# Performance work log

Measured on AMD Instinct MI355X. Metric: run time of the kernel, lower is better.

The kernel has to match this reference:

```python
import jax, jax.numpy as jnp
import numpy as np

D_MODEL = 1024
NUM_HEADS = 16
D_K = D_MODEL // NUM_HEADS


def setup_inputs() -> dict:
    key = jax.random.key(0)
    ks = jax.random.split(key, 16)
    B, S, D = 4, 2048, D_MODEL
    scale = 1.0 / np.sqrt(D)
    inp = {
        'Xs': jax.random.normal(ks[0], (B, S, D), jnp.float32),
        'Xt': jax.random.normal(ks[1], (B, S, D), jnp.float32),
    }
    names = ['qs', 'qt', 'ks', 'kt', 'vs', 'vt']
    for i, n in enumerate(names):
        inp['W_' + n] = jax.random.normal(ks[2 + 2 * i], (D, D), jnp.float32) * scale
        inp['b_' + n] = jax.random.normal(ks[3 + 2 * i], (D,), jnp.float32) * 0.01
    inp['attn_bias'] = jnp.zeros((1, 1, 1, 1), jnp.float32)
    return inp


def _split_heads(x):
    B, S, _ = x.shape
    return x.reshape(B, S, NUM_HEADS, D_K).transpose(0, 2, 1, 3)  # (B,H,S,dk)


def reference(Xs, Xt, W_qs, b_qs, W_qt, b_qt, W_ks, b_ks, W_kt, b_kt,
              W_vs, b_vs, W_vt, b_vt, attn_bias):
    # Dual-linear fused projections: Linear(x) = x @ W.T + b (torch convention)
    Q = Xs @ W_qs.T + b_qs + Xt @ W_qt.T + b_qt
    K = Xs @ W_ks.T + b_ks + Xt @ W_kt.T + b_kt
    V = Xs @ W_vs.T + b_vs + Xt @ W_vt.T + b_vt
    Q, K, V = _split_heads(Q), _split_heads(K), _split_heads(V)
    scores = jnp.einsum('bhqd,bhkd->bhqk', Q, K) / jnp.sqrt(jnp.float32(D_K))
    scores = scores + attn_bias  # scalar learned bias, broadcast
    probs = jax.nn.softmax(scores, axis=-1)
    out = jnp.einsum('bhqk,bhkd->bhqd', probs, V)  # (B,H,S,dk)
    B, H, S, dk = out.shape
    return out.transpose(0, 2, 1, 3).reshape(B, S, H * dk)
```

## Files before the change

kernel.cpp:

```cpp
#include <hip/hip_runtime.h>
#include <hip/hip_bf16.h>

typedef __bf16 bf16;
typedef __attribute__((ext_vector_type(8))) __bf16 bf16x8;
typedef __attribute__((ext_vector_type(4))) __bf16 bf16x4;
typedef __attribute__((ext_vector_type(4))) float f32x4;

#define D_MODEL 1024
#define NHEAD 16
#define DK 64
#define BB 4
#define SS 2048
#define MM 8192
#define KK 2048
#define NN 3072

#define LDP 72
#define QSCALE 0.18033688011112042f

__device__ __forceinline__ void glds16(const bf16* g, bf16* s) {
    __builtin_amdgcn_global_load_lds(
        (const __attribute__((address_space(1))) void*)g,
        (__attribute__((address_space(3))) void*)s, 16, 0, 0);
}

__device__ __forceinline__ void pack_group4(const float* __restrict__ srow,
                                            bf16* __restrict__ dst,
                                            int mt, int ktile, int mi, int g4) {
    const float4* s4 = (const float4*)&srow[g4 * 32];
    bf16x8 o[4];
#pragma unroll
    for (int q = 0; q < 4; ++q) {
        float4 v0 = s4[2 * q], v1 = s4[2 * q + 1];
        o[q][0]=(bf16)v0.x; o[q][1]=(bf16)v0.y; o[q][2]=(bf16)v0.z; o[q][3]=(bf16)v0.w;
        o[q][4]=(bf16)v1.x; o[q][5]=(bf16)v1.y; o[q][6]=(bf16)v1.z; o[q][7]=(bf16)v1.w;
    }
    const int s = mi & 7;
    const int chi = 4 * (g4 & 1);
    bf16* base = dst + (((((size_t)mt * 32 + ktile) << 10) + mi * 8) << 3);
#pragma unroll
    for (int q = 0; q < 4; ++q)
        *(bf16x8*)&base[((q + chi) ^ s) << 3] = o[q];
}

__global__ void pack_all(const float* __restrict__ Xs, const float* __restrict__ Xt,
                         const float* __restrict__ Wqs, const float* __restrict__ Wqt,
                         const float* __restrict__ Wks, const float* __restrict__ Wkt,
                         const float* __restrict__ Wvs, const float* __restrict__ Wvt,
                         const float* __restrict__ bqs, const float* __restrict__ bqt,
                         const float* __restrict__ bks, const float* __restrict__ bkt,
                         const float* __restrict__ bvs, const float* __restrict__ bvt,
                         bf16* __restrict__ Xp, bf16* __restrict__ Wp,
                         float* __restrict__ biasc) {
    int blk = blockIdx.x;
    if (blk < 2048) {
        int u = blk * 256 + threadIdx.x;
        int sel = u >> 18;
        int idx4 = u & 262143;
        int m = idx4 >> 5, g4 = idx4 & 31;
        const float* src = sel ? Xt : Xs;
        pack_group4(src + ((size_t)m << 10), Xp,
                    m >> 7, sel * 16 + (g4 >> 1), m & 127, g4);
        return;
    }
    if (blk < 2816) {
        int v = (blk - 2048) * 256 + threadIdx.x;
        int gi = v >> 15;
        int idx4 = v & 32767;
        int m = idx4 >> 5, g4 = idx4 & 31;
        const float* src = (gi == 0) ? Wqs : (gi == 1) ? Wqt : (gi == 2) ? Wks
                         : (gi == 3) ? Wkt : (gi == 4) ? Wvs : Wvt;
        pack_group4(src + ((size_t)m << 10), Wp,
                    (gi >> 1) * 8 + (m >> 7), (gi & 1) * 16 + (g4 >> 1),
                    m & 127, g4);
        return;
    }
    for (int n = threadIdx.x; n < NN; n += 256) {
        int g = n >> 10, c = n & 1023;
        const float* a = (g == 0) ? bqs : ((g == 1) ? bks : bvs);
        const float* b = (g == 0) ? bqt : ((g == 1) ? bkt : bvt);
        biasc[n] = a[c] + b[c];
    }
}

#define VM6 asm volatile("s_waitcnt vmcnt(6)" ::: "memory")
#define VM0 asm volatile("s_waitcnt vmcnt(0)" ::: "memory")
#define VMNONE
#define LGKM0 asm volatile("s_waitcnt lgkmcnt(0)" ::: "memory")

#define STG(gsrc, ldst) do {                                                  \
    glds16((gsrc) + ((size_t)t << 3), (ldst) + (w << 9));                     \
    glds16((gsrc) + (((size_t)t + 512) << 3), (ldst) + ((w + 8) << 9));       \
  } while (0)

#define TILE(P, KT, DO_STAGE, VMOP) do {                                      \
    const bf16* aP = &sA[P][wm << 6];                                         \
    const bf16* bP = &sB[P][bH][bR << 6];                                     \
    bf16x8 aF[4][2], bF[4][2];                                                \
    _Pragma("unroll")                                                         \
    for (int mi = 0; mi < 4; mi++)                                            \
      aF[mi][0] = *(const bf16x8*)&aP[((mi*16+l16)<<6) + ((quad^swz)<<3)];    \
    _Pragma("unroll")                                                         \
    for (int ni = 0; ni < 4; ni++)                                            \
      bF[ni][0] = *(const bf16x8*)&bP[((ni*16+l16)<<6) + ((quad^swz)<<3)];    \
    _Pragma("unroll")                                                         \
    for (int mi = 0; mi < 4; mi++)                                            \
      aF[mi][1] = *(const bf16x8*)&aP[((mi*16+l16)<<6) + (((4+quad)^swz)<<3)];\
    _Pragma("unroll")                                                         \
    for (int ni = 0; ni < 4; ni++)                                            \
      bF[ni][1] = *(const bf16x8*)&bP[((ni*16+l16)<<6) + (((4+quad)^swz)<<3)];\
    __builtin_amdgcn_s_setprio(1);                                            \
    _Pragma("unroll")                                                         \
    for (int mi = 0; mi < 4; mi++)                                            \
      _Pragma("unroll")                                                       \
      for (int ni = 0; ni < 4; ni++)                                          \
        acc[mi][ni] = __builtin_amdgcn_mfma_f32_16x16x32_bf16(                \
            aF[mi][0], bF[ni][0], acc[mi][ni], 0, 0, 0);                      \
    __builtin_amdgcn_s_setprio(0);                                            \
    LGKM0;                                                                    \
    __builtin_amdgcn_sched_barrier(0);                                        \
    __builtin_amdgcn_s_barrier();                                             \
    __builtin_amdgcn_sched_barrier(0);                                        \
    if (DO_STAGE) {                                                           \
      STG(Ag  + ((size_t)((KT) + 2) << 13), &sA[P][0]);                       \
      STG(Bg0 + ((size_t)((KT) + 2) << 13), &sB[P][0][0]);                    \
      STG(Bg1 + ((size_t)((KT) + 2) << 13), &sB[P][1][0]);                    \
    }                                                                         \
    __builtin_amdgcn_s_setprio(1);                                            \
    _Pragma("unroll")                                                         \
    for (int mi = 0; mi < 4; mi++)                                            \
      _Pragma("unroll")                                                       \
      for (int ni = 0; ni < 4; ni++)                                          \
        acc[mi][ni] = __builtin_amdgcn_mfma_f32_16x16x32_bf16(                \
            aF[mi][1], bF[ni][1], acc[mi][ni], 0, 0, 0);                      \
    __builtin_amdgcn_s_setprio(0);                                            \
    VMOP;                                                                     \
    __builtin_amdgcn_s_barrier();                                             \
    __builtin_amdgcn_sched_barrier(0);                                        \
  } while (0)

__global__ __launch_bounds__(512, 2) void gemm_qkv(
    const bf16* __restrict__ Xp, const bf16* __restrict__ Wp,
    const float* __restrict__ biasc,
    bf16* __restrict__ Qb, bf16* __restrict__ Kb, bf16* __restrict__ Vt) {
    __shared__ __align__(16) bf16 sA[2][8192];
    __shared__ __align__(16) bf16 sB[2][2][8192];

    const int t = threadIdx.x, lane = t & 63, w = t >> 6;
    const int quad = lane >> 4, l16 = lane & 15, swz = l16 & 7;
    const int wq = w & 3;
    const int wm = (w >> 2) * 64;
    const int wn = wq * 64;
    const int bH = wq >> 1;
    const int bR = (wq & 1) * 64;

    const int bx = blockIdx.x, by = blockIdx.y;
    const bf16* Ag  = Xp + (((size_t)bx * 32) << 13);
    const bf16* Bg0 = Wp + (((size_t)(by * 2 + 0) * 32) << 13);
    const bf16* Bg1 = Wp + (((size_t)(by * 2 + 1) * 32) << 13);

    f32x4 acc[4][4] = {};

    STG(Ag, &sA[0][0]); STG(Bg0, &sB[0][0][0]); STG(Bg1, &sB[0][1][0]);
    STG(Ag + 8192, &sA[1][0]); STG(Bg0 + 8192, &sB[1][0][0]); STG(Bg1 + 8192, &sB[1][1][0]);
    VM6;
    __builtin_amdgcn_s_barrier();
    __builtin_amdgcn_sched_barrier(0);

    int kt = 0;
#pragma unroll 1
    for (int i = 0; i < 15; i++, kt += 2) {
        TILE(0, kt, 1, VM6);
        TILE(1, kt + 1, 1, VM6);
    }
    TILE(0, 30, 0, VM0);
    TILE(1, 31, 0, VMNONE);

    const int g = by >> 2;
    const int m00 = bx << 7, n00 = by << 8;
#pragma unroll
    for (int mi = 0; mi < 4; mi++) {
        int mbase = m00 + wm + mi * 16 + quad * 4;
#pragma unroll
        for (int ni = 0; ni < 4; ni++) {
            int n = n00 + wn + ni * 16 + l16;
            float bias = biasc[n];
            int c = n & 1023, h = c >> 6, d = c & 63;
#pragma unroll
            for (int r = 0; r < 4; r++) {
                int m = mbase + r;
                int b = m >> 11, s = m & 2047;
                size_t bh = (size_t)(b * NHEAD + h);
                float v = acc[mi][ni][r] + bias;
                if (g == 0)
                    Qb[(bh * SS + s) * DK + d] = (bf16)(v * QSCALE);
                else if (g == 1)
                    Kb[(bh * SS + s) * DK + d] = (bf16)v;
                else
                    Vt[(bh * DK + d) * SS + s] = (bf16)v;
            }
        }
    }
}

__global__ __launch_bounds__(256) void attn(
    const bf16* __restrict__ Qb, const bf16* __restrict__ Kb,
    const bf16* __restrict__ Vt, float* __restrict__ out) {
    __shared__ __align__(16) bf16 sK[64 * 64];
    __shared__ __align__(16) bf16 sV[64 * 64];
    __shared__ __align__(16) bf16 sP[4][32 * LDP];

    const int lid = blockIdx.x + gridDim.x * blockIdx.y;
    const int bh = (lid & 7) * 8 + ((lid >> 3) & 7);
    const int q0 = (lid >> 6) * 128;

    const int t = threadIdx.x;
    const int lane = t & 63, w = t >> 6;
    const int quad = lane >> 4, l16 = lane & 15, swz = l16 & 7;
    const int b = bh >> 4, h = bh & 15;

    const bf16* Qp = Qb + ((size_t)bh * SS + q0 + w * 32) * DK;
    bf16x8 qf[2][2];
#pragma unroll
    for (int f = 0; f < 2; f++)
#pragma unroll
        for (int kb = 0; kb < 2; kb++)
            qf[f][kb] = *(const bf16x8*)&Qp[(f * 16 + l16) * DK + kb * 32 + quad * 8];

    f32x4 o[2][4] = {};
    float lsum[2] = {0.f, 0.f};

    const bf16* Kp = Kb + (size_t)bh * SS * DK;
    const bf16* Vp = Vt + (size_t)bh * DK * SS;

    for (int kt = 0; kt < SS; kt += 64) {
#pragma unroll
        for (int j = 0; j < 2; j++) {
            int u = (w * 2 + j) * 64 + lane;
            int row = u >> 3;
            int cc = (u & 7) ^ (row & 7);
            glds16(Kp + (size_t)(kt + row) * DK + cc * 8, &sK[(w * 2 + j) * 512]);
            glds16(Vp + (size_t)row * SS + kt + cc * 8, &sV[(w * 2 + j) * 512]);
        }
        __syncthreads();

        f32x4 st[2][4] = {};
#pragma unroll
        for (int kb = 0; kb < 2; kb++)
#pragma unroll
            for (int ki = 0; ki < 4; ki++) {
                bf16x8 kf = *(const bf16x8*)&sK[(ki * 16 + l16) * 64 + (((kb * 4 + quad) ^ swz) * 8)];
                st[0][ki] = __builtin_amdgcn_mfma_f32_16x16x32_bf16(kf, qf[0][kb], st[0][ki], 0, 0, 0);
                st[1][ki] = __builtin_amdgcn_mfma_f32_16x16x32_bf16(kf, qf[1][kb], st[1][ki], 0, 0, 0);
            }

#pragma unroll
        for (int f = 0; f < 2; f++) {
            float ls = 0.f;
#pragma unroll
            for (int ki = 0; ki < 4; ki++) {
                float p0 = __builtin_amdgcn_exp2f(st[f][ki][0]);
                float p1 = __builtin_amdgcn_exp2f(st[f][ki][1]);
                float p2 = __builtin_amdgcn_exp2f(st[f][ki][2]);
                float p3 = __builtin_amdgcn_exp2f(st[f][ki][3]);
                ls += (p0 + p1) + (p2 + p3);
                bf16x4 pk;
                pk[0] = (bf16)p0; pk[1] = (bf16)p1; pk[2] = (bf16)p2; pk[3] = (bf16)p3;
                *(bf16x4*)&sP[w][(f * 16 + l16) * LDP + ki * 16 + quad * 4] = pk;
            }
            lsum[f] += ls;
        }

#pragma unroll
        for (int kb = 0; kb < 2; kb++) {
            bf16x8 af0 = *(const bf16x8*)&sP[w][(l16) * LDP + kb * 32 + quad * 8];
            bf16x8 af1 = *(const bf16x8*)&sP[w][(16 + l16) * LDP + kb * 32 + quad * 8];
#pragma unroll
            for (int ni = 0; ni < 4; ni++) {
                bf16x8 vf = *(const bf16x8*)&sV[(ni * 16 + l16) * 64 + (((kb * 4 + quad) ^ swz) * 8)];
                o[0][ni] = __builtin_amdgcn_mfma_f32_16x16x32_bf16(af0, vf, o[0][ni], 0, 0, 0);
                o[1][ni] = __builtin_amdgcn_mfma_f32_16x16x32_bf16(af1, vf, o[1][ni], 0, 0, 0);
            }
        }
        __syncthreads();
    }

#pragma unroll
    for (int f = 0; f < 2; f++) {
        lsum[f] += __shfl_xor(lsum[f], 16);
        lsum[f] += __shfl_xor(lsum[f], 32);
    }

    float* op = out + ((size_t)(b * SS + q0 + w * 32)) * D_MODEL + h * DK;
#pragma unroll
    for (int f = 0; f < 2; f++)
#pragma unroll
        for (int r = 0; r < 4; r++) {
            float linv = 1.0f / __shfl(lsum[f], quad * 4 + r);
#pragma unroll
            for (int ni = 0; ni < 4; ni++)
                op[(f * 16 + quad * 4 + r) * D_MODEL + ni * 16 + l16] = o[f][ni][r] * linv;
        }
}

extern "C" void kernel_launch(void* const* d_in, const int* in_sizes, int n_in,
                              void* d_out, int out_size, void* d_ws, size_t ws_size,
                              hipStream_t stream) {
    const float* Xs   = (const float*)d_in[0];
    const float* Xt   = (const float*)d_in[1];
    const float* Wqs  = (const float*)d_in[2];
    const float* bqs  = (const float*)d_in[3];
    const float* Wqt  = (const float*)d_in[4];
    const float* bqt  = (const float*)d_in[5];
    const float* Wks  = (const float*)d_in[6];
    const float* bks  = (const float*)d_in[7];
    const float* Wkt  = (const float*)d_in[8];
    const float* bkt  = (const float*)d_in[9];
    const float* Wvs  = (const float*)d_in[10];
    const float* bvs  = (const float*)d_in[11];
    const float* Wvt  = (const float*)d_in[12];
    const float* bvt  = (const float*)d_in[13];
    float* out = (float*)d_out;

    char* ws = (char*)d_ws;
    bf16*  Xp    = (bf16*)(ws);
    bf16*  Wp    = (bf16*)(ws + 33554432);
    float* biasc = (float*)(ws + 46137344);
    bf16*  Qb    = (bf16*)(ws + 46149632);
    bf16*  Kb    = (bf16*)(ws + 62926848);
    bf16*  Vt    = (bf16*)(ws + 79704064);

    pack_all<<<2817, 256, 0, stream>>>(Xs, Xt, Wqs, Wqt, Wks, Wkt, Wvs, Wvt,
                                       bqs, bqt, bks, bkt, bvs, bvt,
                                       Xp, Wp, biasc);

    gemm_qkv<<<dim3(MM / 128, NN / 256), 512, 0, stream>>>(Xp, Wp, biasc, Qb, Kb, Vt);

    attn<<<dim3(SS / 128, BB * NHEAD), 256, 0, stream>>>(Qb, Kb, Vt, out);
}
```

Baseline: 369.8 us.

## Double-buffer K/V tiles in attention kernel to overlap loads with compute

Converts the attention loop's shared K and V tiles to a two-stage ping-pong buffer. The next tile is prefetched with direct-to-LDS global loads while the current tile feeds the MFMAs, and the trailing barrier is replaced by a vmcnt wait plus one barrier per iteration. The goal is to hide global-load latency behind compute. In exchange it doubles K/V LDS usage, which may reduce occupancy, and it depends on a VM0 wait macro defined elsewhere.

Result: slower. 380.9 us (+3.0%).

```diff
diff --git a/kernel.cpp b/kernel.cpp
--- a/kernel.cpp
+++ b/kernel.cpp
@@ -206,8 +206,8 @@
 __global__ __launch_bounds__(256) void attn(
     const bf16* __restrict__ Qb, const bf16* __restrict__ Kb,
     const bf16* __restrict__ Vt, float* __restrict__ out) {
-    __shared__ __align__(16) bf16 sK[64 * 64];
-    __shared__ __align__(16) bf16 sV[64 * 64];
+    __shared__ __align__(16) bf16 sK[2][64 * 64];
+    __shared__ __align__(16) bf16 sV[2][64 * 64];
     __shared__ __align__(16) bf16 sP[4][32 * LDP];
 
     const int lid = blockIdx.x + gridDim.x * blockIdx.y;
@@ -233,23 +233,40 @@
     const bf16* Kp = Kb + (size_t)bh * SS * DK;
     const bf16* Vp = Vt + (size_t)bh * DK * SS;
 
-    for (int kt = 0; kt < SS; kt += 64) {
-#pragma unroll
-        for (int j = 0; j < 2; j++) {
-            int u = (w * 2 + j) * 64 + lane;
-            int row = u >> 3;
-            int cc = (u & 7) ^ (row & 7);
-            glds16(Kp + (size_t)(kt + row) * DK + cc * 8, &sK[(w * 2 + j) * 512]);
-            glds16(Vp + (size_t)row * SS + kt + cc * 8, &sV[(w * 2 + j) * 512]);
-        }
-        __syncthreads();
+    const int u0 = (w * 2 + 0) * 64 + lane, u1 = u0 + 64;
+    const int r0 = u0 >> 3, c0 = (u0 & 7) ^ (r0 & 7);
+    const int r1 = u1 >> 3, c1 = (u1 & 7) ^ (r1 & 7);
+    const bf16* Kg0 = Kp + r0 * DK + c0 * 8;
+    const bf16* Kg1 = Kp + r1 * DK + c1 * 8;
+    const bf16* Vg0 = Vp + (size_t)r0 * SS + c0 * 8;
+    const bf16* Vg1 = Vp + (size_t)r1 * SS + c1 * 8;
+    const int ls0 = (w * 2 + 0) * 512, ls1 = (w * 2 + 1) * 512;
+
+#define ASTG(P, KT) do {                                                      \
+    glds16(Kg0 + (size_t)(KT) * 64, &sK[P][ls0]);                             \
+    glds16(Kg1 + (size_t)(KT) * 64, &sK[P][ls1]);                             \
+    glds16(Vg0 + (KT),              &sV[P][ls0]);                             \
+    glds16(Vg1 + (KT),              &sV[P][ls1]);                             \
+  } while (0)
+
+    ASTG(0, 0);
+
+#pragma unroll 1
+    for (int it = 0; it < 32; ++it) {
+        VM0;
+        __builtin_amdgcn_s_barrier();
+        __builtin_amdgcn_sched_barrier(0);
+        if (it < 31) ASTG((it + 1) & 1, (it + 1) * 64);
+
+        const bf16* kS = &sK[it & 1][0];
+        const bf16* vS = &sV[it & 1][0];
 
         f32x4 st[2][4] = {};
 #pragma unroll
         for (int kb = 0; kb < 2; kb++)
 #pragma unroll
             for (int ki = 0; ki < 4; ki++) {
-                bf16x8 kf = *(const bf16x8*)&sK[(ki * 16 + l16) * 64 + (((kb * 4 + quad) ^ swz) * 8)];
+                bf16x8 kf = *(const bf16x8*)&kS[(ki * 16 + l16) * 64 + (((kb * 4 + quad) ^ swz) * 8)];
                 st[0][ki] = __builtin_amdgcn_mfma_f32_16x16x32_bf16(kf, qf[0][kb], st[0][ki], 0, 0, 0);
                 st[1][ki] = __builtin_amdgcn_mfma_f32_16x16x32_bf16(kf, qf[1][kb], st[1][ki], 0, 0, 0);
             }
@@ -277,13 +294,13 @@
             bf16x8 af1 = *(const bf16x8*)&sP[w][(16 + l16) * LDP + kb * 32 + quad * 8];
 #pragma unroll
             for (int ni = 0; ni < 4; ni++) {
-                bf16x8 vf = *(const bf16x8*)&sV[(ni * 16 + l16) * 64 + (((kb * 4 + quad) ^ swz) * 8)];
+                bf16x8 vf = *(const bf16x8*)&vS[(ni * 16 + l16) * 64 + (((kb * 4 + quad) ^ swz) * 8)];
                 o[0][ni] = __builtin_amdgcn_mfma_f32_16x16x32_bf16(af0, vf, o[0][ni], 0, 0, 0);
                 o[1][ni] = __builtin_amdgcn_mfma_f32_16x16x32_bf16(af1, vf, o[1][ni], 0, 0, 0);
             }
         }
-        __syncthreads();
-    }
+    }
+#undef ASTG
 
 #pragma unroll
     for (int f = 0; f < 2; f++) {
```
